# Performance work log

Hardware: AMD Instinct MI355X
Metric: run time of the kernel (lower is better)

Reference implementation:

```python
import jax, jax.numpy as jnp
import numpy as np

B, T, D, H, O = 64, 2048, 256, 256, 256


def setup_inputs() -> dict:
    key = jax.random.key(0)
    ks = jax.random.split(key, 4)
    s_d = float(1.0 / np.sqrt(D))
    s_h = float(1.0 / np.sqrt(H))
    return {
        "x": jax.random.normal(ks[0], (B, T, D), jnp.float32),
        "c0": jnp.zeros((B, H), jnp.float32),
        "h0": jnp.zeros((B, H), jnp.float32),
        "Wih": jax.random.normal(ks[1], (D, 4 * H), jnp.float32) * s_d,
        "Whh": jax.random.normal(ks[2], (H, 4 * H), jnp.float32) * s_h,
        "bh": jnp.zeros((4 * H,), jnp.float32),
        "Wout": jax.random.normal(ks[3], (H, O), jnp.float32) * s_h,
        "bout": jnp.zeros((O,), jnp.float32),
    }


def reference(x, c0, h0, Wih, Whh, bh, Wout, bout):
    # Teacher-forcing OneToManyRNN: LSTM cell + Dense projection each step.
    # Gate order (flax LSTMCell): i, f, g, o.
    def step(carry, xt):
        c, h = carry
        gates = xt @ Wih + h @ Whh + bh  # [B, 4H]
        i, f, g, o = jnp.split(gates, 4, axis=-1)
        i = jax.nn.sigmoid(i)
        f = jax.nn.sigmoid(f)
        g = jnp.tanh(g)
        o = jax.nn.sigmoid(o)
        c_new = f * c + i * g
        h_new = o * jnp.tanh(c_new)
        y = h_new @ Wout + bout  # dense_out projection
        return (c_new, h_new), y

    xs = jnp.swapaxes(x, 0, 1)  # [T, B, D]
    _, ys = jax.lax.scan(step, (c0, h0), xs)
    return jnp.swapaxes(ys, 0, 1)  # [B, T, O] (stacked per-step outputs)
```

## Files before the change

### kernel.cpp

```cpp
#include <hip/hip_runtime.h>
#include <hip/hip_fp16.h>
#include <cstdint>
#include <cstddef>

typedef _Float16 half_t;
typedef _Float16 half2_t __attribute__((ext_vector_type(2)));
typedef _Float16 half8_t __attribute__((ext_vector_type(8)));
typedef float    f32x4   __attribute__((ext_vector_type(4)));
typedef unsigned int uint4v __attribute__((ext_vector_type(4)));

#define T_FULL  2048
#define T_CH    512
#define N_CHUNK 4
#define B_SZ    64
#define H_SZ    256
#define G4      1024
#define CH_M    (B_SZ * T_CH)

static constexpr size_t OFF_XW   = 0;
static constexpr size_t OFF_H    = OFF_XW   + (size_t)CH_M * G4 * 2;
static constexpr size_t OFF_WIH  = OFF_H    + (size_t)CH_M * H_SZ * 2;
static constexpr size_t OFF_WOUT = OFF_WIH  + (size_t)G4 * 256 * 2;
static constexpr size_t OFF_WMF  = OFF_WOUT + (size_t)256 * 256 * 2;
static constexpr size_t OFF_SC   = OFF_WMF  + (size_t)8 * 64 * 64 * 16;
static constexpr size_t OFF_SH   = OFF_SC   + (size_t)B_SZ * H_SZ * 4;

__device__ __forceinline__ unsigned int packh2(float a, float b) {
    half2_t h; h.x = (half_t)a; h.y = (half_t)b;
    return __builtin_bit_cast(unsigned int, h);
}

__device__ __forceinline__ float sigm(float x)  { return 1.0f / (1.0f + __expf(-x)); }
__device__ __forceinline__ float tanh_(float x) { return 1.0f - 2.0f / (__expf(2.0f * x) + 1.0f); }

static constexpr int PACK_TOTAL = 262144 + 65536 + 131072 + 16384 + 8192;

__global__ __launch_bounds__(256) void pack_kernel(
    const float* __restrict__ Wih, const float* __restrict__ Whh,
    const float* __restrict__ Wout, const float* __restrict__ c0,
    const float* __restrict__ h0,
    half_t* __restrict__ wih_t, half_t* __restrict__ wout_t,
    unsigned int* __restrict__ whh_mf,
    float* __restrict__ state_c, unsigned int* __restrict__ state_h)
{
    const int stride = gridDim.x * blockDim.x;
    for (int idx = blockIdx.x * blockDim.x + threadIdx.x; idx < PACK_TOTAL; idx += stride) {
        int r = idx;
        if (r < 262144) {
            int n = r >> 8, k = r & 255;
            wih_t[r] = (half_t)Wih[k * 1024 + n];
            continue;
        }
        r -= 262144;
        if (r < 65536) {
            int n = r >> 8, k = r & 255;
            wout_t[r] = (half_t)Wout[k * 256 + n];
            continue;
        }
        r -= 65536;
        if (r < 131072) {
            int j    = r & 3;
            int lane = (r >> 2) & 63;
            int nt   = (r >> 8) & 63;
            int kt   = r >> 14;
            int k0 = kt * 32 + ((lane >> 4) << 3) + 2 * j;
            int n  = nt * 16 + (lane & 15);
            whh_mf[r] = packh2(Whh[k0 * 1024 + n], Whh[(k0 + 1) * 1024 + n]);
            continue;
        }
        r -= 131072;
        if (r < 16384) { state_c[r] = c0[r]; continue; }
        r -= 16384;
        state_h[r] = packh2(h0[2 * r], h0[2 * r + 1]);
    }
}

template<int AMODE, int CMODE>
__global__ __launch_bounds__(256) void gemm16(
    const void* __restrict__ Ap, const half_t* __restrict__ Bt,
    void* __restrict__ Cp, const float* __restrict__ bias, int chunk0)
{
    __shared__ half_t Als[128][40];
    __shared__ half_t Bls[128][40];
    const int tid  = threadIdx.x;
    const int lane = tid & 63, wid = tid >> 6;
    const int wr = wid >> 1, wc = wid & 1;
    const int m0 = blockIdx.x * 128, n0 = blockIdx.y * 128;

    f32x4 acc[4][4] = {};

    for (int kc = 0; kc < 8; ++kc) {
        __syncthreads();
        if (AMODE == 1) {
            const float* A = (const float*)Ap;
            #pragma unroll
            for (int i = 0; i < 4; ++i) {
                int l = tid + i * 256;
                int row = l >> 3, kq = l & 7;
                int m = m0 + row;
                int arow = ((m >> 9) << 11) + chunk0 + (m & 511);
                f32x4 v = *(const f32x4*)(A + (size_t)arow * 256 + kc * 32 + kq * 4);
                uint2 pk;
                pk.x = packh2(v.x, v.y);
                pk.y = packh2(v.z, v.w);
                *reinterpret_cast<uint2*>(&Als[row][kq * 4]) = pk;
            }
        } else {
            const half_t* A = (const half_t*)Ap;
            #pragma unroll
            for (int i = 0; i < 2; ++i) {
                int l = tid + i * 256;
                int row = l >> 2, ko = l & 3;
                half8_t v = *(const half8_t*)(A + (size_t)(m0 + row) * 256 + kc * 32 + ko * 8);
                *reinterpret_cast<half8_t*>(&Als[row][ko * 8]) = v;
            }
        }
        #pragma unroll
        for (int i = 0; i < 2; ++i) {
            int l = tid + i * 256;
            int row = l >> 2, ko = l & 3;
            half8_t v = *(const half8_t*)(Bt + (size_t)(n0 + row) * 256 + kc * 32 + ko * 8);
            *reinterpret_cast<half8_t*>(&Bls[row][ko * 8]) = v;
        }
        __syncthreads();

        half8_t af[4], bf[4];
        #pragma unroll
        for (int mi = 0; mi < 4; ++mi)
            af[mi] = *reinterpret_cast<const half8_t*>(&Als[wr * 64 + mi * 16 + (lane & 15)][(lane >> 4) * 8]);
        #pragma unroll
        for (int ni = 0; ni < 4; ++ni)
            bf[ni] = *reinterpret_cast<const half8_t*>(&Bls[wc * 64 + ni * 16 + (lane & 15)][(lane >> 4) * 8]);
        #pragma unroll
        for (int mi = 0; mi < 4; ++mi)
            #pragma unroll
            for (int ni = 0; ni < 4; ++ni)
                acc[mi][ni] = __builtin_amdgcn_mfma_f32_16x16x32_f16(af[mi], bf[ni], acc[mi][ni], 0, 0, 0);
    }

    #pragma unroll
    for (int mi = 0; mi < 4; ++mi) {
        #pragma unroll
        for (int ni = 0; ni < 4; ++ni) {
            #pragma unroll
            for (int reg = 0; reg < 4; ++reg) {
                int row = m0 + wr * 64 + mi * 16 + (lane >> 4) * 4 + reg;
                int col = n0 + wc * 64 + ni * 16 + (lane & 15);
                float v = acc[mi][ni][reg] + bias[col];
                if (CMODE == 0) {
                    ((half_t*)Cp)[(size_t)row * 1024 + ((col & 255) << 2) + (col >> 8)] = (half_t)v;
                } else {
                    int crow = ((row >> 9) << 11) + chunk0 + (row & 511);
                    ((float*)Cp)[(size_t)crow * 256 + col] = v;
                }
            }
        }
    }
}

__global__ __launch_bounds__(512) void rnn_kernel(
    const uint4v* __restrict__ whh_mf,
    const half_t* __restrict__ xw,
    half_t* __restrict__ h_out,
    float* __restrict__ state_c,
    unsigned int* __restrict__ state_h)
{
    __shared__ uint4v lds_b[2 * 4096];
    __shared__ float  gbuf[1024];
    __shared__ unsigned int hbuf[128];

    const int t    = threadIdx.x;
    const int lane = t & 63;
    const int w    = t >> 6;
    const int e    = t & 255;
    const int b    = blockIdx.x;

    for (int i = t; i < 8192; i += 512) lds_b[i] = whh_mf[4 * 4096 + i];
    if (t < 128) hbuf[t] = state_h[b * 128 + t];
    float c = (t < 256) ? state_c[b * 256 + e] : 0.0f;

    const half8_t* mf8 = (const half8_t*)whh_mf;
    half8_t Bres[4][8];
    #pragma unroll
    for (int r = 0; r < 4; ++r)
        #pragma unroll
        for (int ntl = 0; ntl < 8; ++ntl)
            Bres[r][ntl] = mf8[(r * 64 + w * 8 + ntl) * 64 + lane];
    __syncthreads();

    const half_t* xwp = xw + (size_t)b * T_CH * 1024 + e * 4;
    half_t* hop = h_out + (size_t)b * T_CH * 256 + e;
    const half_t* hbh = (const half_t*)hbuf;

    #pragma unroll 1
    for (int step = 0; step < T_CH; ++step) {
        uint2 xv; xv.x = 0; xv.y = 0;
        if (t < 256) xv = *(const uint2*)xwp;

        half8_t a[8];
        #pragma unroll
        for (int kt = 0; kt < 8; ++kt) {
            half8_t v = {};
            if ((lane & 15) == 0)
                v = *(const half8_t*)(hbh + kt * 32 + (lane >> 4) * 8);
            a[kt] = v;
        }

        #pragma unroll
        for (int ntl = 0; ntl < 8; ++ntl) {
            const int nt = w * 8 + ntl;
            half8_t l4 = *(const half8_t*)&lds_b[0 * 4096 + nt * 64 + lane];
            half8_t l5 = *(const half8_t*)&lds_b[1 * 4096 + nt * 64 + lane];
            half8_t g6 = mf8[(6 * 64 + nt) * 64 + lane];
            half8_t g7 = mf8[(7 * 64 + nt) * 64 + lane];
            f32x4 cc = {};
            cc = __builtin_amdgcn_mfma_f32_16x16x32_f16(a[0], Bres[0][ntl], cc, 0, 0, 0);
            cc = __builtin_amdgcn_mfma_f32_16x16x32_f16(a[1], Bres[1][ntl], cc, 0, 0, 0);
            cc = __builtin_amdgcn_mfma_f32_16x16x32_f16(a[2], Bres[2][ntl], cc, 0, 0, 0);
            cc = __builtin_amdgcn_mfma_f32_16x16x32_f16(a[3], Bres[3][ntl], cc, 0, 0, 0);
            cc = __builtin_amdgcn_mfma_f32_16x16x32_f16(a[4], l4, cc, 0, 0, 0);
            cc = __builtin_amdgcn_mfma_f32_16x16x32_f16(a[5], l5, cc, 0, 0, 0);
            cc = __builtin_amdgcn_mfma_f32_16x16x32_f16(a[6], g6, cc, 0, 0, 0);
            cc = __builtin_amdgcn_mfma_f32_16x16x32_f16(a[7], g7, cc, 0, 0, 0);
            if (lane < 16) gbuf[nt * 16 + lane] = cc[0];
        }
        __syncthreads();

        half_t h16 = (half_t)0.f;
        if (t < 256) {
            half2_t x0 = __builtin_bit_cast(half2_t, xv.x);
            half2_t x1 = __builtin_bit_cast(half2_t, xv.y);
            float a0 = gbuf[e]       + (float)x0.x;
            float a1 = gbuf[256 + e] + (float)x0.y;
            float a2 = gbuf[512 + e] + (float)x1.x;
            float a3 = gbuf[768 + e] + (float)x1.y;
            float ig = sigm(a0), fg = sigm(a1), gg = tanh_(a2), og = sigm(a3);
            c = fg * c + ig * gg;
            float hn = og * tanh_(c);
            h16 = (half_t)hn;
            ((half_t*)hbuf)[e] = h16;
        }
        xwp += 1024;
        __syncthreads();

        if (t < 256) *hop = h16;
        hop += 256;
    }

    if (t < 256) state_c[b * 256 + e] = c;
    if (t < 128) state_h[b * 128 + t] = hbuf[t];
}

extern "C" void kernel_launch(void* const* d_in, const int* in_sizes, int n_in,
                              void* d_out, int out_size, void* d_ws, size_t ws_size,
                              hipStream_t stream) {
    const float* x    = (const float*)d_in[0];
    const float* c0   = (const float*)d_in[1];
    const float* h0   = (const float*)d_in[2];
    const float* Wih  = (const float*)d_in[3];
    const float* Whh  = (const float*)d_in[4];
    const float* bh   = (const float*)d_in[5];
    const float* Wout = (const float*)d_in[6];
    const float* bout = (const float*)d_in[7];

    char* ws = (char*)d_ws;
    half_t* xw             = (half_t*)(ws + OFF_XW);
    half_t* h_chunk        = (half_t*)(ws + OFF_H);
    half_t* wih_t          = (half_t*)(ws + OFF_WIH);
    half_t* wout_t         = (half_t*)(ws + OFF_WOUT);
    unsigned int* whh_mf   = (unsigned int*)(ws + OFF_WMF);
    float* state_c         = (float*)(ws + OFF_SC);
    unsigned int* state_h  = (unsigned int*)(ws + OFF_SH);

    pack_kernel<<<512, 256, 0, stream>>>(Wih, Whh, Wout, c0, h0,
                                         wih_t, wout_t, whh_mf,
                                         state_c, state_h);

    for (int ch = 0; ch < N_CHUNK; ++ch) {
        int chunk0 = ch * T_CH;
        gemm16<1, 0><<<dim3(CH_M / 128, G4 / 128), 256, 0, stream>>>(
            (const void*)x, wih_t, (void*)xw, bh, chunk0);
        rnn_kernel<<<B_SZ, 512, 0, stream>>>((const uint4v*)(ws + OFF_WMF),
                                             xw, h_chunk, state_c, state_h);
        gemm16<0, 1><<<dim3(CH_M / 128, H_SZ / 128), 256, 0, stream>>>(
            (const void*)h_chunk, wout_t, d_out, bout, chunk0);
    }
    (void)in_sizes; (void)n_in; (void)out_size; (void)ws_size;
}
```

Baseline: 3.839 ms.

## Keep recurrent weights fully on-chip with 256-thread RNN blocks

```diff
diff --git a/kernel.cpp b/kernel.cpp
--- a/kernel.cpp
+++ b/kernel.cpp
@@ -158,7 +158,9 @@
     }
 }
 
-__global__ __launch_bounds__(512) void rnn_kernel(
+__global__
+__attribute__((amdgpu_flat_work_group_size(256, 256), amdgpu_waves_per_eu(1, 1)))
+void rnn_kernel(
     const uint4v* __restrict__ whh_mf,
     const half_t* __restrict__ xw,
     half_t* __restrict__ h_out,
@@ -172,30 +174,28 @@
     const int t    = threadIdx.x;
     const int lane = t & 63;
     const int w    = t >> 6;
-    const int e    = t & 255;
     const int b    = blockIdx.x;
 
-    for (int i = t; i < 8192; i += 512) lds_b[i] = whh_mf[4 * 4096 + i];
+    for (int i = t; i < 8192; i += 256) lds_b[i] = whh_mf[6 * 4096 + i];
     if (t < 128) hbuf[t] = state_h[b * 128 + t];
-    float c = (t < 256) ? state_c[b * 256 + e] : 0.0f;
+    float c = state_c[b * 256 + t];
 
     const half8_t* mf8 = (const half8_t*)whh_mf;
-    half8_t Bres[4][8];
+    half8_t Bres[6][16];
     #pragma unroll
-    for (int r = 0; r < 4; ++r)
-        #pragma unroll
-        for (int ntl = 0; ntl < 8; ++ntl)
-            Bres[r][ntl] = mf8[(r * 64 + w * 8 + ntl) * 64 + lane];
+    for (int kt = 0; kt < 6; ++kt)
+        #pragma unroll
+        for (int n = 0; n < 16; ++n)
+            Bres[kt][n] = mf8[((size_t)kt * 64 + w * 16 + n) * 64 + lane];
     __syncthreads();
 
-    const half_t* xwp = xw + (size_t)b * T_CH * 1024 + e * 4;
-    half_t* hop = h_out + (size_t)b * T_CH * 256 + e;
+    const half_t* xwp = xw + (size_t)b * T_CH * 1024 + t * 4;
+    half_t* hop = h_out + (size_t)b * T_CH * 256 + t;
     const half_t* hbh = (const half_t*)hbuf;
 
     #pragma unroll 1
     for (int step = 0; step < T_CH; ++step) {
-        uint2 xv; xv.x = 0; xv.y = 0;
-        if (t < 256) xv = *(const uint2*)xwp;
+        uint2 xv = *(const uint2*)xwp;
 
         half8_t a[8];
         #pragma unroll
@@ -207,47 +207,52 @@
         }
 
         #pragma unroll
-        for (int ntl = 0; ntl < 8; ++ntl) {
-            const int nt = w * 8 + ntl;
-            half8_t l4 = *(const half8_t*)&lds_b[0 * 4096 + nt * 64 + lane];
-            half8_t l5 = *(const half8_t*)&lds_b[1 * 4096 + nt * 64 + lane];
-            half8_t g6 = mf8[(6 * 64 + nt) * 64 + lane];
-            half8_t g7 = mf8[(7 * 64 + nt) * 64 + lane];
-            f32x4 cc = {};
-            cc = __builtin_amdgcn_mfma_f32_16x16x32_f16(a[0], Bres[0][ntl], cc, 0, 0, 0);
-            cc = __builtin_amdgcn_mfma_f32_16x16x32_f16(a[1], Bres[1][ntl], cc, 0, 0, 0);
-            cc = __builtin_amdgcn_mfma_f32_16x16x32_f16(a[2], Bres[2][ntl], cc, 0, 0, 0);
-            cc = __builtin_amdgcn_mfma_f32_16x16x32_f16(a[3], Bres[3][ntl], cc, 0, 0, 0);
-            cc = __builtin_amdgcn_mfma_f32_16x16x32_f16(a[4], l4, cc, 0, 0, 0);
-            cc = __builtin_amdgcn_mfma_f32_16x16x32_f16(a[5], l5, cc, 0, 0, 0);
-            cc = __builtin_amdgcn_mfma_f32_16x16x32_f16(a[6], g6, cc, 0, 0, 0);
-            cc = __builtin_amdgcn_mfma_f32_16x16x32_f16(a[7], g7, cc, 0, 0, 0);
-            if (lane < 16) gbuf[nt * 16 + lane] = cc[0];
+        for (int cl = 0; cl < 4; ++cl) {
+            const int nb = w * 16 + cl * 4;
+            half8_t l6[4], l7[4];
+            #pragma unroll
+            for (int i = 0; i < 4; ++i) {
+                l6[i] = *(const half8_t*)&lds_b[0 * 4096 + (size_t)(nb + i) * 64 + lane];
+                l7[i] = *(const half8_t*)&lds_b[1 * 4096 + (size_t)(nb + i) * 64 + lane];
+            }
+            #pragma unroll
+            for (int i = 0; i < 4; ++i) {
+                const int ni = cl * 4 + i;
+                f32x4 cc = {};
+                cc = __builtin_amdgcn_mfma_f32_16x16x32_f16(a[0], Bres[0][ni], cc, 0, 0, 0);
+                cc = __builtin_amdgcn_mfma_f32_16x16x32_f16(a[1], Bres[1][ni], cc, 0, 0, 0);
+                cc = __builtin_amdgcn_mfma_f32_16x16x32_f16(a[2], Bres[2][ni], cc, 0, 0, 0);
+                cc = __builtin_amdgcn_mfma_f32_16x16x32_f16(a[3], Bres[3][ni], cc, 0, 0, 0);
+                cc = __builtin_amdgcn_mfma_f32_16x16x32_f16(a[4], Bres[4][ni], cc, 0, 0, 0);
+                cc = __builtin_amdgcn_mfma_f32_16x16x32_f16(a[5], Bres[5][ni], cc, 0, 0, 0);
+                cc = __builtin_amdgcn_mfma_f32_16x16x32_f16(a[6], l6[i], cc, 0, 0, 0);
+                cc = __builtin_amdgcn_mfma_f32_16x16x32_f16(a[7], l7[i], cc, 0, 0, 0);
+                if (lane < 16) gbuf[(nb + i) * 16 + lane] = cc[0];
+            }
         }
         __syncthreads();
 
-        half_t h16 = (half_t)0.f;
-        if (t < 256) {
+        {
             half2_t x0 = __builtin_bit_cast(half2_t, xv.x);
             half2_t x1 = __builtin_bit_cast(half2_t, xv.y);
-            float a0 = gbuf[e]       + (float)x0.x;
-            float a1 = gbuf[256 + e] + (float)x0.y;
-            float a2 = gbuf[512 + e] + (float)x1.x;
-            float a3 = gbuf[768 + e] + (float)x1.y;
+            float a0 = gbuf[t]       + (float)x0.x;
+            float a1 = gbuf[256 + t] + (float)x0.y;
+            float a2 = gbuf[512 + t] + (float)x1.x;
+            float a3 = gbuf[768 + t] + (float)x1.y;
             float ig = sigm(a0), fg = sigm(a1), gg = tanh_(a2), og = sigm(a3);
             c = fg * c + ig * gg;
             float hn = og * tanh_(c);
-            h16 = (half_t)hn;
-            ((half_t*)hbuf)[e] = h16;
-        }
-        xwp += 1024;
-        __syncthreads();
-
-        if (t < 256) *hop = h16;
-        hop += 256;
-    }
-
-    if (t < 256) state_c[b * 256 + e] = c;
+            half_t h16 = (half_t)hn;
+            ((half_t*)hbuf)[t] = h16;
+            xwp += 1024;
+            __syncthreads();
+
+            *hop = h16;
+            hop += 256;
+        }
+    }
+
+    state_c[b * 256 + t] = c;
     if (t < 128) state_h[b * 128 + t] = hbuf[t];
 }
 
@@ -280,7 +285,7 @@
         int chunk0 = ch * T_CH;
         gemm16<1, 0><<<dim3(CH_M / 128, G4 / 128), 256, 0, stream>>>(
             (const void*)x, wih_t, (void*)xw, bh, chunk0);
-        rnn_kernel<<<B_SZ, 512, 0, stream>>>((const uint4v*)(ws + OFF_WMF),
+        rnn_kernel<<<B_SZ, 256, 0, stream>>>((const uint4v*)(ws + OFF_WMF),
                                              xw, h_chunk, state_c, state_h);
         gemm16<0, 1><<<dim3(CH_M / 128, H_SZ / 128), 256, 0, stream>>>(
             (const void*)h_chunk, wout_t, d_out, bout, chunk0);
```

Measured after the change: 5.310 ms. +38.3%, slower.

## Remap gate tiles per wave so cell update runs in registers, one barrier per step

Applied to the files above, without the earlier changes.

```diff
diff --git a/kernel.cpp b/kernel.cpp
--- a/kernel.cpp
+++ b/kernel.cpp
@@ -158,7 +158,12 @@
     }
 }
 
-__global__ __launch_bounds__(512) void rnn_kernel(
+#define NT(ch) (((ch) < 4) ? (w + 16 * (ch)) : (w + 8 + 16 * ((ch) - 4)))
+#define MFMA16(va, vb, vc) __builtin_amdgcn_mfma_f32_16x16x32_f16((va), (vb), (vc), 0, 0, 0)
+
+__global__
+__attribute__((amdgpu_flat_work_group_size(512, 512), amdgpu_waves_per_eu(2, 2)))
+void rnn_kernel(
     const uint4v* __restrict__ whh_mf,
     const half_t* __restrict__ xw,
     half_t* __restrict__ h_out,
@@ -166,36 +171,39 @@
     unsigned int* __restrict__ state_h)
 {
     __shared__ uint4v lds_b[2 * 4096];
-    __shared__ float  gbuf[1024];
-    __shared__ unsigned int hbuf[128];
+    __shared__ unsigned int hbuf[2][128];
 
     const int t    = threadIdx.x;
     const int lane = t & 63;
     const int w    = t >> 6;
-    const int e    = t & 255;
     const int b    = blockIdx.x;
 
     for (int i = t; i < 8192; i += 512) lds_b[i] = whh_mf[4 * 4096 + i];
-    if (t < 128) hbuf[t] = state_h[b * 128 + t];
-    float c = (t < 256) ? state_c[b * 256 + e] : 0.0f;
+    if (t < 128) hbuf[0][t] = state_h[b * 128 + t];
 
     const half8_t* mf8 = (const half8_t*)whh_mf;
     half8_t Bres[4][8];
     #pragma unroll
-    for (int r = 0; r < 4; ++r)
-        #pragma unroll
-        for (int ntl = 0; ntl < 8; ++ntl)
-            Bres[r][ntl] = mf8[(r * 64 + w * 8 + ntl) * 64 + lane];
+    for (int kt = 0; kt < 4; ++kt)
+        #pragma unroll
+        for (int ch = 0; ch < 8; ++ch)
+            Bres[kt][ch] = mf8[((size_t)kt * 64 + NT(ch)) * 64 + lane];
+
+    const bool upd = (lane < 16);
+    const int e1 = w * 16 + (lane & 15);
+    float c1 = 0.f, c2 = 0.f;
+    if (upd) { c1 = state_c[b * 256 + e1]; c2 = state_c[b * 256 + e1 + 128]; }
+    const half_t* xp  = xw + (size_t)b * T_CH * 1024 + e1 * 4;
+    half_t* hop = h_out + (size_t)b * T_CH * 256 + e1;
     __syncthreads();
 
-    const half_t* xwp = xw + (size_t)b * T_CH * 1024 + e * 4;
-    half_t* hop = h_out + (size_t)b * T_CH * 256 + e;
-    const half_t* hbh = (const half_t*)hbuf;
-
+    int p = 0;
     #pragma unroll 1
     for (int step = 0; step < T_CH; ++step) {
-        uint2 xv; xv.x = 0; xv.y = 0;
-        if (t < 256) xv = *(const uint2*)xwp;
+        const half_t* hbh = (const half_t*)hbuf[p];
+
+        uint2 xv1, xv2; xv1.x = xv1.y = xv2.x = xv2.y = 0;
+        if (upd) { xv1 = *(const uint2*)xp; xv2 = *(const uint2*)(xp + 512); }
 
         half8_t a[8];
         #pragma unroll
@@ -206,49 +214,92 @@
             a[kt] = v;
         }
 
-        #pragma unroll
-        for (int ntl = 0; ntl < 8; ++ntl) {
-            const int nt = w * 8 + ntl;
-            half8_t l4 = *(const half8_t*)&lds_b[0 * 4096 + nt * 64 + lane];
-            half8_t l5 = *(const half8_t*)&lds_b[1 * 4096 + nt * 64 + lane];
-            half8_t g6 = mf8[(6 * 64 + nt) * 64 + lane];
-            half8_t g7 = mf8[(7 * 64 + nt) * 64 + lane];
-            f32x4 cc = {};
-            cc = __builtin_amdgcn_mfma_f32_16x16x32_f16(a[0], Bres[0][ntl], cc, 0, 0, 0);
-            cc = __builtin_amdgcn_mfma_f32_16x16x32_f16(a[1], Bres[1][ntl], cc, 0, 0, 0);
-            cc = __builtin_amdgcn_mfma_f32_16x16x32_f16(a[2], Bres[2][ntl], cc, 0, 0, 0);
-            cc = __builtin_amdgcn_mfma_f32_16x16x32_f16(a[3], Bres[3][ntl], cc, 0, 0, 0);
-            cc = __builtin_amdgcn_mfma_f32_16x16x32_f16(a[4], l4, cc, 0, 0, 0);
-            cc = __builtin_amdgcn_mfma_f32_16x16x32_f16(a[5], l5, cc, 0, 0, 0);
-            cc = __builtin_amdgcn_mfma_f32_16x16x32_f16(a[6], g6, cc, 0, 0, 0);
-            cc = __builtin_amdgcn_mfma_f32_16x16x32_f16(a[7], g7, cc, 0, 0, 0);
-            if (lane < 16) gbuf[nt * 16 + lane] = cc[0];
-        }
+        half8_t s6[8], s7[8];
+        s6[0] = mf8[((size_t)6 * 64 + NT(0)) * 64 + lane];
+        s7[0] = mf8[((size_t)7 * 64 + NT(0)) * 64 + lane];
+        s6[1] = mf8[((size_t)6 * 64 + NT(1)) * 64 + lane];
+        s7[1] = mf8[((size_t)7 * 64 + NT(1)) * 64 + lane];
+
+        float g[8];
+
+        #pragma unroll
+        for (int c = 0; c < 4; ++c) {
+            const int ch0 = 2 * c, ch1 = 2 * c + 1;
+            if (c < 3) {
+                s6[ch0 + 2] = mf8[((size_t)6 * 64 + NT(ch0 + 2)) * 64 + lane];
+                s7[ch0 + 2] = mf8[((size_t)7 * 64 + NT(ch0 + 2)) * 64 + lane];
+                s6[ch1 + 2] = mf8[((size_t)6 * 64 + NT(ch1 + 2)) * 64 + lane];
+                s7[ch1 + 2] = mf8[((size_t)7 * 64 + NT(ch1 + 2)) * 64 + lane];
+            }
+            {
+                half8_t l4 = *(const half8_t*)&lds_b[(size_t)NT(ch0) * 64 + lane];
+                half8_t l5 = *(const half8_t*)&lds_b[4096 + (size_t)NT(ch0) * 64 + lane];
+                f32x4 cc = {};
+                cc = MFMA16(a[0], Bres[0][ch0], cc);
+                cc = MFMA16(a[1], Bres[1][ch0], cc);
+                cc = MFMA16(a[2], Bres[2][ch0], cc);
+                cc = MFMA16(a[3], Bres[3][ch0], cc);
+                cc = MFMA16(a[4], l4, cc);
+                cc = MFMA16(a[5], l5, cc);
+                cc = MFMA16(a[6], s6[ch0], cc);
+                cc = MFMA16(a[7], s7[ch0], cc);
+                g[ch0] = cc[0];
+            }
+            {
+                half8_t l4 = *(const half8_t*)&lds_b[(size_t)NT(ch1) * 64 + lane];
+                half8_t l5 = *(const half8_t*)&lds_b[4096 + (size_t)NT(ch1) * 64 + lane];
+                f32x4 cc = {};
+                cc = MFMA16(a[0], Bres[0][ch1], cc);
+                cc = MFMA16(a[1], Bres[1][ch1], cc);
+                cc = MFMA16(a[2], Bres[2][ch1], cc);
+                cc = MFMA16(a[3], Bres[3][ch1], cc);
+                cc = MFMA16(a[4], l4, cc);
+                cc = MFMA16(a[5], l5, cc);
+                cc = MFMA16(a[6], s6[ch1], cc);
+                cc = MFMA16(a[7], s7[ch1], cc);
+                g[ch1] = cc[0];
+            }
+        }
+
+        half_t h16_1 = (half_t)0.f, h16_2 = (half_t)0.f;
+        if (upd) {
+            half2_t x0 = __builtin_bit_cast(half2_t, xv1.x);
+            half2_t x1 = __builtin_bit_cast(half2_t, xv1.y);
+            float A0 = g[0] + (float)x0.x;
+            float A1 = g[1] + (float)x0.y;
+            float A2 = g[2] + (float)x1.x;
+            float A3 = g[3] + (float)x1.y;
+            float ig = sigm(A0), fg = sigm(A1), gg = tanh_(A2), og = sigm(A3);
+            c1 = fg * c1 + ig * gg;
+            h16_1 = (half_t)(og * tanh_(c1));
+
+            half2_t y0 = __builtin_bit_cast(half2_t, xv2.x);
+            half2_t y1 = __builtin_bit_cast(half2_t, xv2.y);
+            A0 = g[4] + (float)y0.x;
+            A1 = g[5] + (float)y0.y;
+            A2 = g[6] + (float)y1.x;
+            A3 = g[7] + (float)y1.y;
+            ig = sigm(A0); fg = sigm(A1); gg = tanh_(A2); og = sigm(A3);
+            c2 = fg * c2 + ig * gg;
+            h16_2 = (half_t)(og * tanh_(c2));
+
+            half_t* hb = (half_t*)hbuf[p ^ 1];
+            hb[e1]       = h16_1;
+            hb[e1 + 128] = h16_2;
+        }
+        xp += 1024;
         __syncthreads();
 
-        half_t h16 = (half_t)0.f;
-        if (t < 256) {
-            half2_t x0 = __builtin_bit_cast(half2_t, xv.x);
-            half2_t x1 = __builtin_bit_cast(half2_t, xv.y);
-            float a0 = gbuf[e]       + (float)x0.x;
-            float a1 = gbuf[256 + e] + (float)x0.y;
-            float a2 = gbuf[512 + e] + (float)x1.x;
-            float a3 = gbuf[768 + e] + (float)x1.y;
-            float ig = sigm(a0), fg = sigm(a1), gg = tanh_(a2), og = sigm(a3);
-            c = fg * c + ig * gg;
-            float hn = og * tanh_(c);
-            h16 = (half_t)hn;
-            ((half_t*)hbuf)[e] = h16;
-        }
-        xwp += 1024;
-        __syncthreads();
-
-        if (t < 256) *hop = h16;
+        if (upd) { hop[0] = h16_1; hop[128] = h16_2; }
         hop += 256;
-    }
-
-    if (t < 256) state_c[b * 256 + e] = c;
-    if (t < 128) state_h[b * 128 + t] = hbuf[t];
+        p ^= 1;
+    }
+
+    if (upd) {
+        state_c[b * 256 + e1]       = c1;
+        state_c[b * 256 + e1 + 128] = c2;
+    }
+    if (t < 128) state_h[b * 128 + t] = hbuf[p][t];
 }
 
 extern "C" void kernel_launch(void* const* d_in, const int* in_sizes, int n_in,
```

Measured after the change: 5.136 ms. 33.8% more time.
